# Kernel tuning notes

Measured on AMD Instinct MI355X. Metric: run time of the kernel, lower is better.

Reference implementation:

```python
import jax, jax.numpy as jnp
import numpy as np

B, T, D = 4, 2048, 1024  # batch, seq_len, dec_dim_in == dim_proj_QK == dim_proj_V == dec_dim_out


def setup_inputs() -> dict:
    key = jax.random.key(0)
    ks = jax.random.split(key, 9)
    s = 1.0 / np.sqrt(D)  # torch Linear default init scale
    return {
        "x": jax.random.normal(ks[0], (B, T, D), dtype=jnp.float32),
        "Wq": jax.random.uniform(ks[1], (D, D), jnp.float32, -s, s),
        "bq": jax.random.uniform(ks[2], (D,), jnp.float32, -s, s),
        "Wk": jax.random.uniform(ks[3], (D, D), jnp.float32, -s, s),
        "bk": jax.random.uniform(ks[4], (D,), jnp.float32, -s, s),
        "Wv": jax.random.uniform(ks[5], (D, D), jnp.float32, -s, s),
        "bv": jax.random.uniform(ks[6], (D,), jnp.float32, -s, s),
        "Wh": jax.random.uniform(ks[7], (D, D), jnp.float32, -s, s),
        "bh": jax.random.uniform(ks[8], (D,), jnp.float32, -s, s),
    }


def reference(x, Wq, bq, Wk, bk, Wv, bv, Wh, bh):
    Q = x @ Wq + bq                      # [B, T, Dqk]
    K = x @ Wk + bk                      # [B, T, Dqk]
    V = x @ Wv + bv                      # [B, T, Dv]
    scale = 1.0 / jnp.sqrt(jnp.asarray(K.shape[-1], x.dtype))
    scores = jnp.einsum("btd,bsd->bts", Q, K) * scale  # [B, T, T]
    t = K.shape[1]
    causal = jnp.triu(jnp.ones((t, t), dtype=bool), k=1)  # True above diagonal
    scores = jnp.where(causal[None, :, :], -jnp.inf, scores)
    attn = jax.nn.softmax(scores, axis=-1)
    # dropout is identity in eval mode (reference baseline)
    out = jnp.einsum("bts,bsd->btd", attn, V)  # [B, T, Dv]
    return out @ Wh + bh
```

## Files before the change

kernel.cpp:

```cpp
#include <hip/hip_runtime.h>


typedef __attribute__((ext_vector_type(8)))  short short8;
typedef __attribute__((ext_vector_type(4)))  float f4;

#define BM 128
#define BN 128
#define BK 64
#define BM2 256
#define BN2 256
#define BM3 128
#define BN3 256

#define F_OBF    1
#define F_SKIP   2
#define F_KLIM   4
#define F_REVY   8
#define F_VSPL   16
#define F_RSCL   32
#define F_EXP    64
#define F_RSUM   128
#define F_SPLITK 256

#define WAITV4() asm volatile("s_waitcnt vmcnt(4)" ::: "memory")
#define WAITV6() asm volatile("s_waitcnt vmcnt(6)" ::: "memory")
#define WAITV8() asm volatile("s_waitcnt vmcnt(8)" ::: "memory")
#define WAITV0() asm volatile("s_waitcnt vmcnt(0)" ::: "memory")
#define SBAR()   __builtin_amdgcn_s_barrier()
#define PRIO1()  __builtin_amdgcn_s_setprio(1)
#define PRIO0()  __builtin_amdgcn_s_setprio(0)

__device__ inline unsigned short f2bf(float f) {
    union { float f; unsigned u; } c; c.f = f;
    unsigned u = c.u;
    return (unsigned short)((u + 0x7fffu + ((u >> 16) & 1u)) >> 16);
}
__device__ inline float bf2f(unsigned short u) {
    union { unsigned u; float f; } c; c.u = ((unsigned)u) << 16;
    return c.f;
}
__device__ inline void gload16(const void* g, void* l) {
    __builtin_amdgcn_global_load_lds(
        (const __attribute__((address_space(1))) void*)g,
        (__attribute__((address_space(3))) void*)l,
        16, 0, 0);
}

template<int FLAGS>
__global__ __launch_bounds__(256)
void gemm_bt(const unsigned short* __restrict__ A,
             const unsigned short* __restrict__ Bt,
             void* __restrict__ C,
             const float* __restrict__ bias,
             int M, int N, int K, int lda, int ldb, int ldc,
             long sA, long sB, long sC,
             float scale,
             unsigned short* __restrict__ C2, long sC2, int Tv, int vsplit,
             float* __restrict__ rowsums)
{
    const int b = blockIdx.z;
    A  += (long)b * sA;
    Bt += (long)b * sB;

    int by = blockIdx.y;
    if (FLAGS & F_REVY) by = gridDim.y - 1 - by;
    const int m0 = by * BM;
    const int n0 = blockIdx.x * BN;

    const int kt1 = K / BK;

    __shared__ unsigned short As[BM * BK];
    __shared__ unsigned short Bs[BN * BK];

    const int tid  = threadIdx.x;
    const int lane = tid & 63;
    const int wave = tid >> 6;
    const int wm   = wave & 1;
    const int wn   = wave >> 1;
    const int lrow = lane & 15;
    const int quad = lane >> 4;

    f4 acc[4][4];
#pragma unroll
    for (int i = 0; i < 4; ++i)
#pragma unroll
        for (int j = 0; j < 4; ++j) acc[i][j] = (f4)0.0f;

    const int srow = tid >> 3;
    const int gco  = ((tid & 7) ^ (srow & 7)) << 3;
    const int rdsl = (lrow & 7);

    for (int kt = 0; kt < kt1; ++kt) {
        const int k0 = kt * BK;
#pragma unroll
        for (int d = 0; d < 4; ++d) {
            const int row = d * 32 + srow;
            const unsigned short* ga = A  + (long)(m0 + row) * lda + k0 + gco;
            const unsigned short* gb = Bt + (long)(n0 + row) * ldb + k0 + gco;
            const int ldsoff = (d * 256 + wave * 64) * 16;
            gload16(ga, (char*)As + ldsoff);
            gload16(gb, (char*)Bs + ldsoff);
        }
        __syncthreads();

#pragma unroll
        for (int ks = 0; ks < 2; ++ks) {
            const int slot = ((ks * 4 + quad) ^ rdsl) << 3;
            short8 af[4], bfr[4];
#pragma unroll
            for (int i = 0; i < 4; ++i) {
                af[i]  = *(const short8*)(As + (wm * 64 + i * 16 + lrow) * BK + slot);
                bfr[i] = *(const short8*)(Bs + (wn * 64 + i * 16 + lrow) * BK + slot);
            }
#pragma unroll
            for (int i = 0; i < 4; ++i)
#pragma unroll
                for (int j = 0; j < 4; ++j)
                    acc[i][j] = __builtin_amdgcn_mfma_f32_16x16x32_bf16(
                        af[i], bfr[j], acc[i][j], 0, 0, 0);
        }
        __syncthreads();
    }

    const int row0 = m0 + wm * 64 + quad * 4;
    const int col0 = n0 + wn * 64 + lrow;

    float bj[4];
#pragma unroll
    for (int j = 0; j < 4; ++j) bj[j] = bias ? bias[col0 + j * 16] : 0.0f;

    unsigned short* Cb = (unsigned short*)C;
    float*          Cf = (float*)C;
    const long cbase = (long)b * sC;

#pragma unroll
    for (int i = 0; i < 4; ++i) {
#pragma unroll
        for (int j = 0; j < 4; ++j) {
            const int col = col0 + j * 16;
#pragma unroll
            for (int r = 0; r < 4; ++r) {
                const int row = row0 + i * 16 + r;
                float v = acc[i][j][r] * scale + bj[j];
                const long off = cbase + (long)row * ldc + col;
                if (FLAGS & F_OBF) Cb[off] = f2bf(v);
                else               Cf[off] = v;
            }
        }
    }
}

template<int QB>
__device__ inline void ldb_q(short8 (&bq)[4], const unsigned short* Bsb,
                             int wn, int lrow, int quad, int rdsl)
{
#pragma unroll
    for (int j = 0; j < 2; ++j)
#pragma unroll
        for (int ks = 0; ks < 2; ++ks)
            bq[j * 2 + ks] = *(const short8*)(
                Bsb + (wn * 64 + QB * 32 + j * 16 + lrow) * BK
                    + (((ks * 4 + quad) ^ rdsl) << 3));
}

template<int ND>
__device__ inline void stage_mat(const unsigned short* __restrict__ Row,
                                 int k0, unsigned short* Ls, int ld, int tid)
{
    const int srow = tid >> 3;
    const int gco  = ((tid & 7) ^ (srow & 7)) << 3;
    const int wave = tid >> 6;
#pragma unroll
    for (int d = 0; d < ND; ++d) {
        const int row = d * 64 + srow;
        const int ldsoff = (d * 512 + wave * 64) * 16;
        gload16(Row + (long)row * ld + k0 + gco, (char*)Ls + ldsoff);
    }
}

template<int HA>
__device__ inline void lda_half(short8 (&af)[8], const unsigned short* Asb,
                                int wm, int lrow, int quad, int rdsl)
{
#pragma unroll
    for (int i = 0; i < 4; ++i)
#pragma unroll
        for (int ks = 0; ks < 2; ++ks)
            af[i * 2 + ks] = *(const short8*)(
                Asb + (wm * 128 + HA * 64 + i * 16 + lrow) * BK
                    + (((ks * 4 + quad) ^ rdsl) << 3));
}

template<int RI, int CJ>
__device__ inline void mfma_cl(f4 (&acc)[8][4], const short8 (&a)[8],
                               const short8 (&b)[4])
{
#pragma unroll
    for (int ks = 0; ks < 2; ++ks)
#pragma unroll
        for (int i = 0; i < 4; ++i)
#pragma unroll
            for (int j = 0; j < 2; ++j)
                acc[RI + i][CJ + j] = __builtin_amdgcn_mfma_f32_16x16x32_bf16(
                    a[i * 2 + ks], b[j * 2 + ks], acc[RI + i][CJ + j], 0, 0, 0);
}

__device__ inline void lda_w(short8 (&af)[8], const unsigned short* Asb,
                             int wm, int lrow, int quad, int rdsl)
{
#pragma unroll
    for (int i = 0; i < 4; ++i)
#pragma unroll
        for (int ks = 0; ks < 2; ++ks)
            af[i * 2 + ks] = *(const short8*)(
                Asb + (wm * 64 + i * 16 + lrow) * BK
                    + (((ks * 4 + quad) ^ rdsl) << 3));
}

template<int CJ>
__device__ inline void mfma16(f4 (&acc)[4][4], const short8 (&a)[8],
                              const short8 (&b)[4])
{
#pragma unroll
    for (int ks = 0; ks < 2; ++ks)
#pragma unroll
        for (int i = 0; i < 4; ++i)
#pragma unroll
            for (int j = 0; j < 2; ++j)
                acc[i][CJ + j] = __builtin_amdgcn_mfma_f32_16x16x32_bf16(
                    a[i * 2 + ks], b[j * 2 + ks], acc[i][CJ + j], 0, 0, 0);
}

template<int FLAGS, int GX = 0, int GY = 0>
__global__ __launch_bounds__(512)
void gemm256(const unsigned short* __restrict__ A,
             const unsigned short* __restrict__ Bt,
             void* __restrict__ C,
             const float* __restrict__ bias,
             int M, int N, int K, int lda, int ldb, int ldc,
             long sA, long sB, long sC,
             float scale,
             unsigned short* __restrict__ C2, long sC2, int Tv, int vsplit,
             float* __restrict__ rowsums)
{
    const int b = blockIdx.z;
    A  += (long)b * sA;
    Bt += (long)b * sB;
    if (FLAGS & (F_RSCL | F_RSUM)) rowsums += (long)b * M;

    int bxr = blockIdx.x, byr = blockIdx.y;
    if (GX > 0) {
        constexpr int NWG = GX * GY;
        constexpr int Q   = NWG >> 3;
        static_assert((NWG & 7) == 0, "swizzle needs NWG%8==0");
        const int lin  = byr * GX + bxr;
        const int virt = (lin & 7) * Q + (lin >> 3);
        bxr = virt % GX; byr = virt / GX;
    }

    int by = byr;
    if (FLAGS & F_REVY) by = gridDim.y - 1 - by;
    const int m0 = by * BM2;

    int n0, split = 0;
    if (FLAGS & F_SPLITK) {
        const int nbx = N / BN2;
        n0 = (bxr % nbx) * BN2;
        split = bxr / nbx;
        if (split && m0 < 1024) return;
    } else {
        n0 = bxr * BN2;
    }

    if ((FLAGS & F_SKIP) && n0 > m0 + (BM2 - 1)) return;

    int kend = K;
    if (FLAGS & F_KLIM) { int ke = m0 + BM2; kend = ke < K ? ke : K; }
    int kt0 = 0;
    if (FLAGS & F_SPLITK) {
        if (split == 0) { if (kend > 1024) kend = 1024; }
        else            { kt0 = 1024 / BK; }
    }
    const int kt1 = kend / BK;

    __shared__ unsigned short sm[4][BM2 * BK];

    const int tid  = threadIdx.x;
    const int lane = tid & 63;
    const int wave = tid >> 6;
    const int wm   = wave & 1;
    const int wn   = wave >> 1;
    const int lrow = lane & 15;
    const int quad = lane >> 4;
    const int rdsl = lrow & 7;

    f4 acc[8][4];
#pragma unroll
    for (int i = 0; i < 8; ++i)
#pragma unroll
        for (int j = 0; j < 4; ++j) acc[i][j] = (f4)0.0f;

    const unsigned short* Arow = A  + (long)m0 * lda;
    const unsigned short* Brow = Bt + (long)n0 * ldb;
    const int ktiles = kt1 - kt0;

    short8 af[8], bg0[4], bg1[4];

    stage_mat<4>(Arow, kt0 * BK, sm[0], lda, tid);
    stage_mat<4>(Brow, kt0 * BK, sm[1], ldb, tid);
    stage_mat<4>(Arow, (kt0 + 1) * BK, sm[2], lda, tid);
    stage_mat<4>(Brow, (kt0 + 1) * BK, sm[3], ldb, tid);
    WAITV8();
    SBAR();
    lda_half<0>(af, sm[0], wm, lrow, quad, rdsl);
    ldb_q<0>(bg0, sm[1], wn, lrow, quad, rdsl);

    for (int t = 0; t < ktiles; ++t) {
        const int cur = t & 1;
        const unsigned short* Asb = sm[cur * 2];
        const unsigned short* Bsb = sm[cur * 2 + 1];
        const bool s2 = (t + 2 < ktiles);
        const bool rd = (t + 1 < ktiles);

        PRIO1(); mfma_cl<0, 0>(acc, af, bg0); PRIO0();
        ldb_q<1>(bg1, Bsb, wn, lrow, quad, rdsl);
        SBAR();

        PRIO1(); mfma_cl<0, 2>(acc, af, bg1); PRIO0();
        lda_half<1>(af, Asb, wm, lrow, quad, rdsl);
        SBAR();

        PRIO1(); mfma_cl<4, 2>(acc, af, bg1); PRIO0();
        if (s2) { stage_mat<4>(Arow, (kt0 + t + 2) * BK, sm[cur * 2], lda, tid);
                  WAITV4(); }
        else    { WAITV0(); }
        SBAR();

        if (s2) stage_mat<4>(Brow, (kt0 + t + 2) * BK, sm[cur * 2 + 1], ldb, tid);
        PRIO1(); mfma_cl<4, 0>(acc, af, bg0); PRIO0();
        if (rd) {
            const unsigned short* An = sm[(cur ^ 1) * 2];
            const unsigned short* Bn = sm[(cur ^ 1) * 2 + 1];
            lda_half<0>(af, An, wm, lrow, quad, rdsl);
            ldb_q<0>(bg0, Bn, wn, lrow, quad, rdsl);
        }
        SBAR();
    }

    const int row0 = m0 + wm * 128 + quad * 4;
    const int col0 = n0 + wn * 64 + lrow;

    float bj[4];
#pragma unroll
    for (int j = 0; j < 4; ++j) bj[j] = bias ? bias[col0 + j * 16] : 0.0f;

    if ((FLAGS & F_VSPL) && n0 >= vsplit) {
        const int bidx  = m0 >> 11;
        const int tloc0 = (m0 & 2047) + wm * 128 + quad * 4;
#pragma unroll
        for (int j = 0; j < 4; ++j) {
            const int d = col0 + j * 16 - vsplit;
            unsigned short* base = C2 + (long)bidx * sC2 + (long)d * Tv;
#pragma unroll
            for (int i = 0; i < 8; ++i) {
                const int tt = tloc0 + i * 16;
                unsigned long long pk = 0;
#pragma unroll
                for (int r = 0; r < 4; ++r) {
                    float v = acc[i][j][r] * scale + bj[j];
                    pk |= (unsigned long long)f2bf(v) << (16 * r);
                }
                *(unsigned long long*)(base + tt) = pk;
            }
        }
        return;
    }

    float inv[32];
    if (FLAGS & F_RSCL) {
#pragma unroll
        for (int i = 0; i < 8; ++i)
#pragma unroll
            for (int r = 0; r < 4; ++r)
                inv[i * 4 + r] = rowsums[row0 + i * 16 + r];
    }

    float rs[32];
    if (FLAGS & F_RSUM) {
#pragma unroll
        for (int k = 0; k < 32; ++k) rs[k] = 0.0f;
    }

    unsigned short* Cb = (unsigned short*)C;
    float*          Cf = ((FLAGS & F_SPLITK) && split) ? (float*)C2 : (float*)C;
    const long cbase = (long)b * sC;

#pragma unroll
    for (int i = 0; i < 8; ++i) {
#pragma unroll
        for (int j = 0; j < 4; ++j) {
            const int col = col0 + j * 16;
#pragma unroll
            for (int r = 0; r < 4; ++r) {
                const int row = row0 + i * 16 + r;
                float v = acc[i][j][r] * scale;
                if (FLAGS & F_EXP) { v = __expf(v); if (col > row) v = 0.0f; }
                if (FLAGS & F_RSUM) rs[i * 4 + r] += v;
                if (FLAGS & F_RSCL) v *= inv[i * 4 + r];
                if (!((FLAGS & F_SPLITK) && split)) v += bj[j];
                const long off = cbase + (long)row * ldc + col;
                if (FLAGS & F_OBF) Cb[off] = f2bf(v);
                else               Cf[off] = v;
            }
        }
    }

    if (FLAGS & F_RSUM) {
#pragma unroll
        for (int k = 0; k < 32; ++k) {
            rs[k] += __shfl_xor(rs[k], 1);
            rs[k] += __shfl_xor(rs[k], 2);
            rs[k] += __shfl_xor(rs[k], 4);
            rs[k] += __shfl_xor(rs[k], 8);
        }
        if (lrow == 0) {
#pragma unroll
            for (int i = 0; i < 8; ++i)
#pragma unroll
                for (int r = 0; r < 4; ++r)
                    atomicAdd(&rowsums[row0 + i * 16 + r], rs[i * 4 + r]);
        }
    }
}

template<int FLAGS, int GX = 0, int GY = 0>
__global__ __launch_bounds__(512)
void gemmw(const unsigned short* __restrict__ A,
           const unsigned short* __restrict__ Bt,
           void* __restrict__ C,
           const float* __restrict__ bias,
           int M, int N, int K, int lda, int ldb, int ldc,
           long sA, long sB, long sC,
           float scale,
           unsigned short* __restrict__ C2, long sC2, int Tv, int vsplit,
           float* __restrict__ rowsums)
{
    const int b = blockIdx.z;
    A  += (long)b * sA;
    Bt += (long)b * sB;

    int bxr = blockIdx.x, byr = blockIdx.y;
    if (GX > 0) {
        constexpr int NWG = GX * GY;
        constexpr int Q   = NWG >> 3;
        static_assert((NWG & 7) == 0, "swizzle needs NWG%8==0");
        const int lin  = byr * GX + bxr;
        const int virt = (lin & 7) * Q + (lin >> 3);
        bxr = virt % GX; byr = virt / GX;
    }

    const int m0 = byr * BM3;
    const int n0 = bxr * BN3;
    const int kt1 = K / BK;

    __shared__ unsigned short smA[2][BM3 * BK];
    __shared__ unsigned short smB[2][BN3 * BK];

    const int tid  = threadIdx.x;
    const int lane = tid & 63;
    const int wave = tid >> 6;
    const int wm   = wave & 1;
    const int wn   = wave >> 1;
    const int lrow = lane & 15;
    const int quad = lane >> 4;
    const int rdsl = lrow & 7;

    f4 acc[4][4];
#pragma unroll
    for (int i = 0; i < 4; ++i)
#pragma unroll
        for (int j = 0; j < 4; ++j) acc[i][j] = (f4)0.0f;

    const unsigned short* Arow = A  + (long)m0 * lda;
    const unsigned short* Brow = Bt + (long)n0 * ldb;
    const int ktiles = kt1;

    short8 af[8], bg0[4], bg1[4];

    stage_mat<2>(Arow, 0, smA[0], lda, tid);
    stage_mat<4>(Brow, 0, smB[0], ldb, tid);
    stage_mat<2>(Arow, BK, smA[1], lda, tid);
    stage_mat<4>(Brow, BK, smB[1], ldb, tid);
    WAITV6();
    SBAR();
    lda_w(af, smA[0], wm, lrow, quad, rdsl);
    ldb_q<0>(bg0, smB[0], wn, lrow, quad, rdsl);

    for (int t = 0; t < ktiles; ++t) {
        const int cur = t & 1;
        const bool s2 = (t + 2 < ktiles);
        const bool rd = (t + 1 < ktiles);

        PRIO1(); mfma16<0>(acc, af, bg0); PRIO0();
        ldb_q<1>(bg1, smB[cur], wn, lrow, quad, rdsl);
        SBAR();

        PRIO1(); mfma16<2>(acc, af, bg1); PRIO0();
        if (s2) {
            stage_mat<2>(Arow, (t + 2) * BK, smA[cur], lda, tid);
            stage_mat<4>(Brow, (t + 2) * BK, smB[cur], ldb, tid);
            WAITV6();
        } else {
            WAITV0();
        }
        SBAR();
        if (rd) {
            lda_w(af, smA[cur ^ 1], wm, lrow, quad, rdsl);
            ldb_q<0>(bg0, smB[cur ^ 1], wn, lrow, quad, rdsl);
        }
    }

    const int row0 = m0 + wm * 64 + quad * 4;
    const int col0 = n0 + wn * 64 + lrow;

    float bj[4];
#pragma unroll
    for (int j = 0; j < 4; ++j) bj[j] = bias ? bias[col0 + j * 16] : 0.0f;

    if ((FLAGS & F_VSPL) && n0 >= vsplit) {
        const int bidx  = m0 >> 11;
        const int tloc0 = (m0 & 2047) + wm * 64 + quad * 4;
#pragma unroll
        for (int j = 0; j < 4; ++j) {
            const int d = col0 + j * 16 - vsplit;
            unsigned short* base = C2 + (long)bidx * sC2 + (long)d * Tv;
#pragma unroll
            for (int i = 0; i < 4; ++i) {
                const int tt = tloc0 + i * 16;
                unsigned long long pk = 0;
#pragma unroll
                for (int r = 0; r < 4; ++r) {
                    float v = acc[i][j][r] * scale + bj[j];
                    pk |= (unsigned long long)f2bf(v) << (16 * r);
                }
                *(unsigned long long*)(base + tt) = pk;
            }
        }
        return;
    }

    unsigned short* Cb = (unsigned short*)C;
    float*          Cf = (float*)C;
    const long cbase = (long)b * sC;

#pragma unroll
    for (int i = 0; i < 4; ++i) {
#pragma unroll
        for (int j = 0; j < 4; ++j) {
            const int col = col0 + j * 16;
#pragma unroll
            for (int r = 0; r < 4; ++r) {
                const int row = row0 + i * 16 + r;
                float v = acc[i][j][r] * scale + bj[j];
                const long off = cbase + (long)row * ldc + col;
                if (FLAGS & F_OBF) Cb[off] = f2bf(v);
                else               Cf[off] = v;
            }
        }
    }
}

__global__ void combine_upper(float* __restrict__ out,
                              const float* __restrict__ part)
{
    const long base = ((long)blockIdx.y * 2048 + 1024) * 1024 / 4;
    const long i = base + blockIdx.x * 256 + threadIdx.x;
    f4 a = ((f4*)out)[i];
    f4 bb = ((const f4*)part)[i];
    a.x += bb.x; a.y += bb.y; a.z += bb.z; a.w += bb.w;
    ((f4*)out)[i] = a;
}

__global__ void recip_sums(float* __restrict__ s)
{
    const int i = blockIdx.x * 256 + threadIdx.x;
    s[i] = 1.0f / s[i];
}

__global__ void gemv_bhh(const unsigned short* __restrict__ Wht,
                         const float* __restrict__ bv,
                         const float* __restrict__ bh,
                         float* __restrict__ bhh)
{
    const int m = blockIdx.x;
    const int tid = threadIdx.x;
    const int lane = tid & 63, wave = tid >> 6;
    __shared__ float red[4];
    const unsigned short* row = Wht + (long)m * 1024;
    float s = 0.0f;
#pragma unroll
    for (int k = 0; k < 4; ++k) {
        const int idx = tid * 4 + k;
        s += bf2f(row[idx]) * bv[idx];
    }
    for (int o = 32; o > 0; o >>= 1) s += __shfl_down(s, o);
    if (lane == 0) red[wave] = s;
    __syncthreads();
    if (tid == 0) bhh[m] = red[0] + red[1] + red[2] + red[3] + bh[m];
}

__global__ void prep(const float* __restrict__ x,
                     const float* __restrict__ Wq, const float* __restrict__ Wk,
                     const float* __restrict__ Wv, const float* __restrict__ Wh,
                     const float* __restrict__ bq, const float* __restrict__ bk,
                     unsigned short* __restrict__ Xbf,
                     unsigned short* __restrict__ Wqkvt,
                     unsigned short* __restrict__ Wht,
                     unsigned short* __restrict__ Wvb,
                     float* __restrict__ bqkv)
{
    __shared__ unsigned short tsh[32][33];
    const int bid = blockIdx.x;
    const int tid = threadIdx.x;

    if (bid < 8192) {
        const int i = bid * 256 + tid;
        f4 v = ((const f4*)x)[i];
        unsigned long long p = (unsigned long long)f2bf(v.x)
                             | ((unsigned long long)f2bf(v.y) << 16)
                             | ((unsigned long long)f2bf(v.z) << 32)
                             | ((unsigned long long)f2bf(v.w) << 48);
        ((unsigned long long*)Xbf)[i] = p;
    } else if (bid < 9216) {
        const int i = (bid - 8192) * 256 + tid;
        f4 v = ((const f4*)Wv)[i];
        unsigned long long p = (unsigned long long)f2bf(v.x)
                             | ((unsigned long long)f2bf(v.y) << 16)
                             | ((unsigned long long)f2bf(v.z) << 32)
                             | ((unsigned long long)f2bf(v.w) << 48);
        ((unsigned long long*)Wvb)[i] = p;
    } else if (bid < 12288) {
        const int wi = bid - 9216;
        const int w = wi >> 10, tile = wi & 1023;
        const float* src = (w == 0) ? Wq : (w == 1) ? Wk : Wh;
        unsigned short* dst = (w == 0) ? Wqkvt : (w == 1) ? (Wqkvt + 1024 * 1024) : Wht;
        const int c0 = (tile & 31) * 32, r0 = (tile >> 5) * 32;
        const int xx = tid & 31, yy = tid >> 5;
        for (int i = yy; i < 32; i += 8)
            tsh[i][xx] = f2bf(src[(long)(r0 + i) * 1024 + c0 + xx]);
        __syncthreads();
        for (int i = yy; i < 32; i += 8)
            dst[(long)(c0 + i) * 1024 + r0 + xx] = tsh[xx][i];
    } else {
        const int i = (bid - 12288) * 256 + tid;
        if (i < 1024) { bqkv[i] = bq[i]; bqkv[1024 + i] = bk[i]; bqkv[2048 + i] = 0.0f; }
    }
}

extern "C" void kernel_launch(void* const* d_in, const int* in_sizes, int n_in,
                              void* d_out, int out_size, void* d_ws, size_t ws_size,
                              hipStream_t stream)
{
    const float* x  = (const float*)d_in[0];
    const float* Wq = (const float*)d_in[1];
    const float* bq = (const float*)d_in[2];
    const float* Wk = (const float*)d_in[3];
    const float* bk = (const float*)d_in[4];
    const float* Wv = (const float*)d_in[5];
    const float* bv = (const float*)d_in[6];
    const float* Wh = (const float*)d_in[7];
    const float* bh = (const float*)d_in[8];
    float* out = (float*)d_out;

    const int  Bb = 4, T = 2048, Dm = 1024;
    const long BT = (long)Bb * T;

    unsigned short* ws = (unsigned short*)d_ws;
    size_t o = 0;
    unsigned short* Xbf   = ws + o; o += (size_t)BT * Dm;
    unsigned short* Wqkvt = ws + o; o += (size_t)3 * Dm * Dm;
    unsigned short* Wht   = ws + o; o += (size_t)Dm * Dm;
    unsigned short* Wvb   = ws + o; o += (size_t)Dm * Dm;
    float* bqkv = (float*)(ws + o); o += (size_t)3 * Dm * 2;
    float* bhh  = (float*)(ws + o); o += (size_t)Dm * 2;
    float* sums = (float*)(ws + o); o += (size_t)BT * 2;
    unsigned short* QKV   = ws + o; o += (size_t)BT * 3 * Dm;
    unsigned short* Vt    = ws + o; o += (size_t)BT * Dm;
    unsigned short* Pp    = ws + o; o += (size_t)Bb * T * T;
    float* part = (float*)(ws + o);

    const dim3 blk(256);
    const dim3 blk2(512);
    const long sRow3 = (long)T * 3 * Dm;

    hipMemsetAsync(sums, 0, (size_t)BT * sizeof(float), stream);

    prep<<<12289, blk, 0, stream>>>(x, Wq, Wk, Wv, Wh, bq, bk,
                                    Xbf, Wqkvt, Wht, Wvb, bqkv);

    gemm_bt<F_OBF><<<dim3(Dm / BN, Dm / BM, 1), blk, 0, stream>>>(
        Wht, Wvb, Wqkvt + 2 * Dm * Dm, nullptr, Dm, Dm, Dm, Dm, Dm, Dm,
        0, 0, 0, 1.0f, nullptr, 0, 0, 0, nullptr);

    gemv_bhh<<<Dm, blk, 0, stream>>>(Wht, bv, bh, bhh);

    gemm256<F_OBF, 8, 32>
        <<<dim3(2 * Dm / BN2, BT / BM2, 1), blk2, 0, stream>>>(
        Xbf, Wqkvt, QKV, bqkv, (int)BT, 2 * Dm, Dm, Dm, Dm, 3 * Dm,
        0, 0, 0, 1.0f, nullptr, 0, 0, 0, nullptr);

    gemmw<F_OBF | F_VSPL, 4, 64>
        <<<dim3(Dm / BN3, BT / BM3, 1), blk2, 0, stream>>>(
        Xbf, Wqkvt + 2 * Dm * Dm, QKV, nullptr, (int)BT, Dm, Dm, Dm, Dm, 3 * Dm,
        0, 0, 0, 1.0f, Vt, (long)Dm * T, T, 0, nullptr);

    gemm256<F_OBF | F_SKIP | F_REVY | F_EXP | F_RSUM, 8, 8>
        <<<dim3(T / BN2, T / BM2, Bb), blk2, 0, stream>>>(
        QKV, QKV + Dm, Pp, nullptr, T, T, Dm, 3 * Dm, 3 * Dm, T,
        sRow3, sRow3, (long)T * T, 1.0f / 32.0f,
        nullptr, 0, 0, 0, sums);

    recip_sums<<<dim3((int)(BT / 256)), blk, 0, stream>>>(sums);

    gemm256<F_KLIM | F_REVY | F_RSCL | F_SPLITK, 8, 8>
        <<<dim3(2 * Dm / BN2, T / BM2, Bb), blk2, 0, stream>>>(
        Pp, Vt, out, bhh, T, Dm, T, T, T, Dm,
        (long)T * T, (long)Dm * T, (long)T * Dm, 1.0f,
        (unsigned short*)part, 0, 0, 0, sums);

    combine_upper<<<dim3(1024, Bb), blk, 0, stream>>>(out, part);
}
```

Baseline: 274.6 us.

## Compute transposed scores tile to write packed bf16 and cut row-sum atomics

The score GEMM now computes K·Qᵀ (operands swapped) and writes each output transposed back into P's row-major layout. The transpose makes the four consecutive accumulator values in a lane contiguous, so they go out as one 64-bit store instead of scattered 16-bit stores, and row sums need far fewer shuffles and atomics. The separate memset and reciprocal kernels are folded into the prep kernel and the PV epilogue, removing two launches. The change risks uncoalesced column-strided stores across lanes and a different causal skip and scheduling order, since REVY was dropped.

```diff
diff --git a/kernel.cpp b/kernel.cpp
--- a/kernel.cpp
+++ b/kernel.cpp
@@ -21,6 +21,7 @@
 #define F_EXP    64
 #define F_RSUM   128
 #define F_SPLITK 256
+#define F_TRS    512
 
 #define WAITV4() asm volatile("s_waitcnt vmcnt(4)" ::: "memory")
 #define WAITV6() asm volatile("s_waitcnt vmcnt(6)" ::: "memory")
@@ -272,7 +273,10 @@
         n0 = bxr * BN2;
     }
 
-    if ((FLAGS & F_SKIP) && n0 > m0 + (BM2 - 1)) return;
+    if (FLAGS & F_SKIP) {
+        if (FLAGS & F_TRS) { if (m0 > n0 + (BM2 - 1)) return; }
+        else               { if (n0 > m0 + (BM2 - 1)) return; }
+    }
 
     int kend = K;
     if (FLAGS & F_KLIM) { int ke = m0 + BM2; kend = ke < K ? ke : K; }
@@ -350,6 +354,44 @@
     const int row0 = m0 + wm * 128 + quad * 4;
     const int col0 = n0 + wn * 64 + lrow;
 
+    unsigned short* Cb = (unsigned short*)C;
+    const long cbase = (long)b * sC;
+
+    if (FLAGS & F_TRS) {
+        float rsj[4];
+#pragma unroll
+        for (int j = 0; j < 4; ++j) rsj[j] = 0.0f;
+#pragma unroll
+        for (int j = 0; j < 4; ++j) {
+            const int col = col0 + j * 16;
+#pragma unroll
+            for (int i = 0; i < 8; ++i) {
+                unsigned long long pk = 0;
+#pragma unroll
+                for (int r = 0; r < 4; ++r) {
+                    const int row = row0 + i * 16 + r;
+                    float v = __expf(acc[i][j][r] * scale);
+                    if (row > col) v = 0.0f;
+                    rsj[j] += v;
+                    pk |= (unsigned long long)f2bf(v) << (16 * r);
+                }
+                *(unsigned long long*)(Cb + cbase + (long)col * ldc
+                                       + row0 + i * 16) = pk;
+            }
+        }
+#pragma unroll
+        for (int j = 0; j < 4; ++j) {
+            rsj[j] += __shfl_xor(rsj[j], 16);
+            rsj[j] += __shfl_xor(rsj[j], 32);
+        }
+        if (quad == 0) {
+#pragma unroll
+            for (int j = 0; j < 4; ++j)
+                atomicAdd(&rowsums[col0 + j * 16], rsj[j]);
+        }
+        return;
+    }
+
     float bj[4];
 #pragma unroll
     for (int j = 0; j < 4; ++j) bj[j] = bias ? bias[col0 + j * 16] : 0.0f;
@@ -382,18 +424,10 @@
         for (int i = 0; i < 8; ++i)
 #pragma unroll
             for (int r = 0; r < 4; ++r)
-                inv[i * 4 + r] = rowsums[row0 + i * 16 + r];
-    }
-
-    float rs[32];
-    if (FLAGS & F_RSUM) {
-#pragma unroll
-        for (int k = 0; k < 32; ++k) rs[k] = 0.0f;
-    }
-
-    unsigned short* Cb = (unsigned short*)C;
+                inv[i * 4 + r] = 1.0f / rowsums[row0 + i * 16 + r];
+    }
+
     float*          Cf = ((FLAGS & F_SPLITK) && split) ? (float*)C2 : (float*)C;
-    const long cbase = (long)b * sC;
 
 #pragma unroll
     for (int i = 0; i < 8; ++i) {
@@ -404,31 +438,12 @@
             for (int r = 0; r < 4; ++r) {
                 const int row = row0 + i * 16 + r;
                 float v = acc[i][j][r] * scale;
-                if (FLAGS & F_EXP) { v = __expf(v); if (col > row) v = 0.0f; }
-                if (FLAGS & F_RSUM) rs[i * 4 + r] += v;
                 if (FLAGS & F_RSCL) v *= inv[i * 4 + r];
                 if (!((FLAGS & F_SPLITK) && split)) v += bj[j];
                 const long off = cbase + (long)row * ldc + col;
                 if (FLAGS & F_OBF) Cb[off] = f2bf(v);
                 else               Cf[off] = v;
             }
-        }
-    }
-
-    if (FLAGS & F_RSUM) {
-#pragma unroll
-        for (int k = 0; k < 32; ++k) {
-            rs[k] += __shfl_xor(rs[k], 1);
-            rs[k] += __shfl_xor(rs[k], 2);
-            rs[k] += __shfl_xor(rs[k], 4);
-            rs[k] += __shfl_xor(rs[k], 8);
-        }
-        if (lrow == 0) {
-#pragma unroll
-            for (int i = 0; i < 8; ++i)
-#pragma unroll
-                for (int r = 0; r < 4; ++r)
-                    atomicAdd(&rowsums[row0 + i * 16 + r], rs[i * 4 + r]);
         }
     }
 }
@@ -581,12 +596,6 @@
     ((f4*)out)[i] = a;
 }
 
-__global__ void recip_sums(float* __restrict__ s)
-{
-    const int i = blockIdx.x * 256 + threadIdx.x;
-    s[i] = 1.0f / s[i];
-}
-
 __global__ void gemv_bhh(const unsigned short* __restrict__ Wht,
                          const float* __restrict__ bv,
                          const float* __restrict__ bh,
@@ -617,7 +626,8 @@
                      unsigned short* __restrict__ Wqkvt,
                      unsigned short* __restrict__ Wht,
                      unsigned short* __restrict__ Wvb,
-                     float* __restrict__ bqkv)
+                     float* __restrict__ bqkv,
+                     float* __restrict__ sums)
 {
     __shared__ unsigned short tsh[32][33];
     const int bid = blockIdx.x;
@@ -654,6 +664,7 @@
     } else {
         const int i = (bid - 12288) * 256 + tid;
         if (i < 1024) { bqkv[i] = bq[i]; bqkv[1024 + i] = bk[i]; bqkv[2048 + i] = 0.0f; }
+        for (int k = tid; k < 8192; k += 256) sums[k] = 0.0f;
     }
 }
 
@@ -693,10 +704,8 @@
     const dim3 blk2(512);
     const long sRow3 = (long)T * 3 * Dm;
 
-    hipMemsetAsync(sums, 0, (size_t)BT * sizeof(float), stream);
-
     prep<<<12289, blk, 0, stream>>>(x, Wq, Wk, Wv, Wh, bq, bk,
-                                    Xbf, Wqkvt, Wht, Wvb, bqkv);
+                                    Xbf, Wqkvt, Wht, Wvb, bqkv, sums);
 
     gemm_bt<F_OBF><<<dim3(Dm / BN, Dm / BM, 1), blk, 0, stream>>>(
         Wht, Wvb, Wqkvt + 2 * Dm * Dm, nullptr, Dm, Dm, Dm, Dm, Dm, Dm,
@@ -714,13 +723,11 @@
         Xbf, Wqkvt + 2 * Dm * Dm, QKV, nullptr, (int)BT, Dm, Dm, Dm, Dm, 3 * Dm,
         0, 0, 0, 1.0f, Vt, (long)Dm * T, T, 0, nullptr);
 
-    gemm256<F_OBF | F_SKIP | F_REVY | F_EXP | F_RSUM, 8, 8>
+    gemm256<F_OBF | F_SKIP | F_EXP | F_RSUM | F_TRS, 8, 8>
         <<<dim3(T / BN2, T / BM2, Bb), blk2, 0, stream>>>(
-        QKV, QKV + Dm, Pp, nullptr, T, T, Dm, 3 * Dm, 3 * Dm, T,
+        QKV + Dm, QKV, Pp, nullptr, T, T, Dm, 3 * Dm, 3 * Dm, T,
         sRow3, sRow3, (long)T * T, 1.0f / 32.0f,
         nullptr, 0, 0, 0, sums);
-
-    recip_sums<<<dim3((int)(BT / 256)), blk, 0, stream>>>(sums);
 
     gemm256<F_KLIM | F_REVY | F_RSCL | F_SPLITK, 8, 8>
         <<<dim3(2 * Dm / BN2, T / BM2, Bb), blk2, 0, stream>>>(
```

Measured after the change: 270.4 us. About the same (-1.5%).
